# Kernel optimization log

Measured on AMD Instinct MI355X. Metric: run time of the kernel, lower is better.

The kernel has to match this reference:

```python
import jax, jax.numpy as jnp
import numpy as np

B, N, C = 4, 4096, 64
K1, K2 = 4, 6
MLP1 = [128, 64, 64]
MLP2 = [128, 64]
EPS = 1e-5


def _sqdist(a, b):
    # a: [B,N,3], b: [B,M,3] -> [B,N,M]
    return (jnp.sum(a * a, -1)[:, :, None] + jnp.sum(b * b, -1)[:, None, :]
            - 2.0 * jnp.einsum('bnc,bmc->bnm', a, b))


def _knn_idx(k, xyz, new_xyz):
    # matches knn_point: topk of -square_distance(new_xyz, xyz)
    _, idx = jax.lax.top_k(-_sqdist(new_xyz, xyz), k)
    return idx  # [B,S,k]


def _gather(points, idx):
    # index_points: points [B,N,C], idx [B,S,K] -> [B,S,K,C]
    return jax.vmap(lambda p, i: p[i])(points, idx)


def _conv_bn_relu(x, w, g, b):
    # 1x1 Conv2d (no bias) + BatchNorm2d (train mode) + ReLU, channels-last
    y = jnp.einsum('bnkc,oc->bnko', x, w)
    m = jnp.mean(y, axis=(0, 1, 2), keepdims=True)
    v = jnp.var(y, axis=(0, 1, 2), keepdims=True)
    return jax.nn.relu((y - m) * jax.lax.rsqrt(v + EPS) * g + b)


def _quat_mul(a, b):
    # Hamilton product, matches mul_q_point ordering
    aw, ax, ay, az = a[..., 0], a[..., 1], a[..., 2], a[..., 3]
    bw, bx, by, bz = b[..., 0], b[..., 1], b[..., 2], b[..., 3]
    return jnp.stack([
        aw * bw - ax * bx - ay * by - az * bz,
        aw * bx + ax * bw + ay * bz - az * by,
        aw * by - ax * bz + ay * bw + az * bx,
        aw * bz + ax * by - ay * bx + az * bw], axis=-1)


def _inv_q(q):
    n2 = jnp.sum(q * q, -1, keepdims=True) + 1e-10
    return jnp.concatenate([q[..., :1], -q[..., 1:]], -1) / n2


def _qrot(q, v):
    # rotate points v [B,M,3] by quaternion q [B,4] via q * (0,v) * q^-1
    vq = jnp.concatenate([jnp.zeros(v.shape[:-1] + (1,), v.dtype), v], -1)
    qb = q[:, None, :]
    return _quat_mul(_quat_mul(qb, vq), _inv_q(q)[:, None, :])[..., 1:]


def setup_inputs() -> dict:
    key = jax.random.key(0)
    ks = jax.random.split(key, 32)

    def rn(i, shape, s=1.0):
        return jax.random.normal(ks[i], shape, jnp.float32) * s

    inp = {
        'pos1': rn(0, (B, N, 3)),
        'pos2': rn(1, (B, N, 3)),
        'feat1': rn(2, (B, N, C)),
        'feat2': rn(3, (B, N, C)),
        'q_coarse': rn(4, (B, 4)),
        't_coarse': rn(5, (B, 3)),
    }
    c1 = [2 * C + 3] + MLP1
    for i in range(len(MLP1)):
        inp['w1_%d' % i] = rn(6 + i, (c1[i + 1], c1[i]), 0.1)
        inp['g1_%d' % i] = jnp.ones((c1[i + 1],), jnp.float32)
        inp['b1_%d' % i] = jnp.zeros((c1[i + 1],), jnp.float32)
    c2 = [MLP1[-1] + C + 3] + MLP2
    for i in range(len(MLP2)):
        inp['w2_%d' % i] = rn(12 + i, (c2[i + 1], c2[i]), 0.1)
        inp['g2_%d' % i] = jnp.ones((c2[i + 1],), jnp.float32)
        inp['b2_%d' % i] = jnp.zeros((c2[i + 1],), jnp.float32)
    inp['wq'] = rn(20, (4, MLP2[-1]), 0.01)
    inp['bq'] = jnp.zeros((4,), jnp.float32)
    inp['wt'] = rn(21, (3, MLP2[-1]), 0.01)
    inp['bt'] = jnp.zeros((3,), jnp.float32)
    return inp


def reference(pos1, pos2, feat1, feat2, q_coarse, t_coarse,
              w1_0, g1_0, b1_0, w1_1, g1_1, b1_1, w1_2, g1_2, b1_2,
              w2_0, g2_0, b2_0, w2_1, g2_1, b2_1, wq, bq, wt, bt):
    # warp pos1 by the coarse pose (q, t)
    pos1_w = _qrot(q_coarse, pos1) + t_coarse[:, None, :]

    # cross-cloud KNN grouping (FlowEmbedding first stage)
    idx2 = _knn_idx(K2, pos2, pos1_w)                      # [B,N,K2]
    xd2 = _gather(pos2, idx2) - pos1_w[:, :, None, :]      # [B,N,K2,3]
    f2g = _gather(feat2, idx2)                             # [B,N,K2,C]
    f1r = jnp.broadcast_to(feat1[:, :, None, :], (B, N, K2, C))
    x = jnp.concatenate([xd2, f2g, f1r], -1)               # [B,N,K2,131]
    for w, g, b in ((w1_0, g1_0, b1_0), (w1_1, g1_1, b1_1), (w1_2, g1_2, b1_2)):
        x = _conv_bn_relu(x, w, g, b)
    fe = jnp.sum(x, axis=2)                                # [B,N,64] sum pool over neighbors

    # self KNN grouping (FlowEmbedding second stage)
    idx1 = _knn_idx(K1, pos1_w, pos1_w)                    # [B,N,K1]
    xd1 = _gather(pos1_w, idx1) - pos1_w[:, :, None, :]
    feg = _gather(fe, idx1)
    f1r2 = jnp.broadcast_to(feat1[:, :, None, :], (B, N, K1, C))
    x = jnp.concatenate([xd1, feg, f1r2], -1)              # [B,N,K1,131]
    for w, g, b in ((w2_0, g2_0, b2_0), (w2_1, g2_1, b2_1)):
        x = _conv_bn_relu(x, w, g, b)
    pooled = jnp.sum(jnp.sum(x, axis=2), axis=1)           # [B,64] sum pool

    # pose delta heads + quaternion composition
    q_det = pooled @ wq.T + bq
    q_det = q_det / (jnp.linalg.norm(q_det, axis=-1, keepdims=True) + 1e-10)
    t_det = pooled @ wt.T + bt
    q_new = _quat_mul(q_det, q_coarse)
    q_new = q_new / (jnp.linalg.norm(q_new, axis=-1, keepdims=True) + 1e-10)
    t_new = _qrot(q_det, t_coarse[:, None, :])[:, 0, :] + t_det
    return jnp.concatenate([q_new, t_new], -1)             # [B,7]
```

## Files before the change

### kernel.cpp

```cpp
#include <hip/hip_runtime.h>
#include <math.h>

#define B_ 4
#define N_ 4096
#define C_ 64
#define K1_ 4
#define K2_ 6
#define EPS_ 1e-5f
#define BN_ (B_ * N_)
#define NCH_ 16
#define CHP_ 256
#define STKD_ 16

typedef __attribute__((ext_vector_type(8))) short bf16x8;
typedef __attribute__((ext_vector_type(4))) float f32x4;
typedef __attribute__((ext_vector_type(2))) float f32x2;

__device__ __forceinline__ unsigned short f2bf(float f) {
  unsigned int u = __float_as_uint(f);
  unsigned int r = (u + 0x7fffu + ((u >> 16) & 1u)) >> 16;
  return (unsigned short)r;
}
__device__ __forceinline__ float bf2f(unsigned short u) {
  return __uint_as_float(((unsigned int)u) << 16);
}

__global__ __launch_bounds__(256) void k_init(
    const float* __restrict__ w1_0, const float* __restrict__ w1_1,
    const float* __restrict__ w1_2, const float* __restrict__ w2_0,
    const float* __restrict__ w2_1, unsigned short* __restrict__ Wf2a,
    unsigned short* __restrict__ Wf1a, unsigned short* __restrict__ Wfe,
    unsigned short* __restrict__ Wf1b, unsigned short* __restrict__ wb1,
    unsigned short* __restrict__ wb2, unsigned short* __restrict__ wb4,
    const float* __restrict__ pos1, const float* __restrict__ pos2,
    const float* __restrict__ qc, const float* __restrict__ tc,
    float* __restrict__ posw, float4* __restrict__ pts4w, float4* __restrict__ pairW,
    float4* __restrict__ pairP) {
  int t = blockIdx.x * 256 + threadIdx.x;
  int m = blockIdx.y;
  if (m < 7) {
    switch (m) {
      case 0:
        if (t < 8192) Wf2a[t] = f2bf(w1_0[(t >> 6) * 131 + 3 + (t & 63)]);
        break;
      case 1:
        if (t < 8192) Wf1a[t] = f2bf(w1_0[(t >> 6) * 131 + 67 + (t & 63)]);
        break;
      case 2:
        if (t < 8192) Wfe[t] = f2bf(w2_0[(t >> 6) * 131 + 3 + (t & 63)]);
        break;
      case 3:
        if (t < 8192) Wf1b[t] = f2bf(w2_0[(t >> 6) * 131 + 67 + (t & 63)]);
        break;
      case 4:
        if (t < 8192) wb1[t] = f2bf(w1_1[t]);
        break;
      case 5:
        if (t < 4096) wb2[t] = f2bf(w1_2[t]);
        break;
      default:
        if (t < 8192) wb4[t] = f2bf(w2_1[t]);
        break;
    }
    return;
  }
  if (t >= BN_) return;
  int b = t / N_;
  float qw = qc[b * 4 + 0], qx = qc[b * 4 + 1], qy = qc[b * 4 + 2], qz = qc[b * 4 + 3];
  float vx = pos1[t * 3 + 0], vy = pos1[t * 3 + 1], vz = pos1[t * 3 + 2];
  float aw = -(qx * vx + qy * vy + qz * vz);
  float ax = qw * vx + qy * vz - qz * vy;
  float ay = qw * vy - qx * vz + qz * vx;
  float az = qw * vz + qx * vy - qy * vx;
  float n2 = qw * qw + qx * qx + qy * qy + qz * qz + 1e-10f;
  float bw = qw / n2, bx = -qx / n2, by = -qy / n2, bz = -qz / n2;
  float rx = aw * bx + ax * bw + ay * bz - az * by;
  float ry = aw * by - ax * bz + ay * bw + az * bx;
  float rz = aw * bz + ax * by - ay * bx + az * bw;
  rx += tc[b * 3 + 0];
  ry += tc[b * 3 + 1];
  rz += tc[b * 3 + 2];
  posw[t * 3 + 0] = rx;
  posw[t * 3 + 1] = ry;
  posw[t * 3 + 2] = rz;
  float rw2 = rx * rx + ry * ry + rz * rz;
  pts4w[t] = make_float4(rx, ry, rz, rw2);
  int p = t >> 1, h = t & 1;
  float* bwp = (float*)&pairW[(size_t)2 * p];
  bwp[0 + h] = rx; bwp[2 + h] = ry; bwp[4 + h] = rz; bwp[6 + h] = rw2;
  float px = pos2[t * 3 + 0], py = pos2[t * 3 + 1], pz = pos2[t * 3 + 2];
  float pw2 = px * px + py * py + pz * pz;
  float* bpp = (float*)&pairP[(size_t)2 * p];
  bpp[0 + h] = px; bpp[2 + h] = py; bpp[4 + h] = pz; bpp[6 + h] = pw2;
}

__device__ __forceinline__ void ins6i(int (&kd)[6], int k) {
  int x = k;
#pragma unroll
  for (int u = 0; u < 6; ++u) {
    int lo = min(kd[u], x);
    x = max(kd[u], x);
    kd[u] = lo;
  }
}

__global__ __launch_bounds__(256) void k_knn2(const float4* __restrict__ pts4w,
                                              const float4* __restrict__ pairW,
                                              const float4* __restrict__ pairP,
                                              int* __restrict__ outK) {
  __shared__ int st[STKD_][256];
  int tid = threadIdx.x;
  int b = blockIdx.z & 3;
  int which = blockIdx.z >> 2;
  const f32x4* __restrict__ PT =
      (const f32x4*)((which ? pairW : pairP) + (size_t)b * N_ + blockIdx.y * CHP_);
  int base = blockIdx.y * CHP_;
  int n = blockIdx.x * 256 + tid;
  float4 qv = pts4w[(size_t)b * N_ + n];
  f32x2 qq2 = (f32x2)(qv.w);
  f32x2 m2x = (f32x2)(-2.f * qv.x);
  f32x2 m2y = (f32x2)(-2.f * qv.y);
  f32x2 m2z = (f32x2)(-2.f * qv.z);
  int kd[6];
#pragma unroll
  for (int t = 0; t < 6; ++t) kd[t] = 0x7fffffff;
  int kbd5 = 0x7fffffff;
  int ptr = 0;
  for (int jj = 0; jj < CHP_; jj += 4) {
    f32x4 e0 = PT[jj + 0];
    f32x4 e1 = PT[jj + 1];
    f32x4 e2 = PT[jj + 2];
    f32x4 e3 = PT[jj + 3];
    f32x2 d01 = __builtin_elementwise_fma(
        m2x, e0.xy,
        __builtin_elementwise_fma(m2y, e0.zw,
                                  __builtin_elementwise_fma(m2z, e1.xy, e1.zw + qq2)));
    f32x2 d23 = __builtin_elementwise_fma(
        m2x, e2.xy,
        __builtin_elementwise_fma(m2y, e2.zw,
                                  __builtin_elementwise_fma(m2z, e3.xy, e3.zw + qq2)));
    int j0 = base + jj;
    int k0 = (int)((__float_as_uint(d01.x) & 0xFFFFF000u) | (unsigned)(j0 + 0));
    int k1 = (int)((__float_as_uint(d01.y) & 0xFFFFF000u) | (unsigned)(j0 + 1));
    int k2 = (int)((__float_as_uint(d23.x) & 0xFFFFF000u) | (unsigned)(j0 + 2));
    int k3 = (int)((__float_as_uint(d23.y) & 0xFFFFF000u) | (unsigned)(j0 + 3));
    st[ptr][tid] = k0;
    ptr += (k0 < kbd5) ? 1 : 0;
    st[ptr][tid] = k1;
    ptr += (k1 < kbd5) ? 1 : 0;
    st[ptr][tid] = k2;
    ptr += (k2 < kbd5) ? 1 : 0;
    st[ptr][tid] = k3;
    ptr += (k3 < kbd5) ? 1 : 0;
    if (__ballot(ptr >= STKD_ - 4)) {
      for (int i = 0; i < ptr; ++i) ins6i(kd, st[i][tid]);
      ptr = 0;
      kbd5 = kd[5];
    }
  }
  for (int i = 0; i < ptr; ++i) ins6i(kd, st[i][tid]);
  size_t ob =
      ((size_t)which * BN_ * NCH_ + (size_t)(b * N_ + n) * NCH_ + blockIdx.y) * 6;
#pragma unroll
  for (int t = 0; t < 6; ++t) outK[ob + t] = kd[t];
}

__global__ __launch_bounds__(64) void k_knn2_merge(const int* __restrict__ inK,
                                                   int* __restrict__ idx2,
                                                   int* __restrict__ idx1) {
  int t = blockIdx.x * 64 + threadIdx.x;
  if (t >= 2 * BN_) return;
  int which = (t >= BN_) ? 1 : 0;
  int qi = t - which * BN_;
  int kd[6];
#pragma unroll
  for (int u = 0; u < 6; ++u) kd[u] = 0x7fffffff;
  size_t ib = ((size_t)which * BN_ + qi) * NCH_ * 6;
  for (int c = 0; c < NCH_ * 6; ++c) ins6i(kd, inK[ib + c]);
  if (which) {
#pragma unroll
    for (int u = 0; u < K1_; ++u) idx1[(size_t)qi * K1_ + u] = kd[u] & 0xFFF;
  } else {
#pragma unroll
    for (int u = 0; u < K2_; ++u) idx2[(size_t)qi * K2_ + u] = kd[u] & 0xFFF;
  }
}

__device__ __forceinline__ void proj_mfma_tail(const unsigned short* Xs, int tid,
                                               int row0,
                                               const unsigned short* __restrict__ Wb,
                                               float* __restrict__ dst) {
  constexpr int SP = 72;
  int l = tid & 63, wv = tid >> 6;
  int lm = l & 15, quad = l >> 4;
  int n0 = wv * 32;
  f32x4 acc[4][2];
#pragma unroll
  for (int rt = 0; rt < 4; ++rt)
#pragma unroll
    for (int ct = 0; ct < 2; ++ct) acc[rt][ct] = (f32x4)(0.f);
#pragma unroll
  for (int k0 = 0; k0 < 64; k0 += 32) {
    bf16x8 a[4], b[2];
#pragma unroll
    for (int rt = 0; rt < 4; ++rt)
      a[rt] = *(const bf16x8*)&Xs[(rt * 16 + lm) * SP + k0 + quad * 8];
#pragma unroll
    for (int ct = 0; ct < 2; ++ct)
      b[ct] = *(const bf16x8*)&Wb[(size_t)(n0 + ct * 16 + lm) * 64 + k0 + quad * 8];
#pragma unroll
    for (int rt = 0; rt < 4; ++rt)
#pragma unroll
      for (int ct = 0; ct < 2; ++ct)
        acc[rt][ct] =
            __builtin_amdgcn_mfma_f32_16x16x32_bf16(a[rt], b[ct], acc[rt][ct], 0, 0, 0);
  }
#pragma unroll
  for (int rt = 0; rt < 4; ++rt)
#pragma unroll
    for (int ct = 0; ct < 2; ++ct)
#pragma unroll
      for (int r = 0; r < 4; ++r) {
        int row = row0 + rt * 16 + quad * 4 + r;
        dst[(size_t)row * 128 + n0 + ct * 16 + lm] = acc[rt][ct][r];
      }
}

__global__ __launch_bounds__(256) void k_proj(
    const float* __restrict__ s0, const unsigned short* __restrict__ w0,
    float* __restrict__ d0, const float* __restrict__ s1,
    const unsigned short* __restrict__ w1, float* __restrict__ d1,
    const float* __restrict__ s2, const unsigned short* __restrict__ w2,
    float* __restrict__ d2) {
  const float* src;
  const unsigned short* Wb;
  float* dst;
  switch (blockIdx.y) {
    case 0: src = s0; Wb = w0; dst = d0; break;
    case 1: src = s1; Wb = w1; dst = d1; break;
    default: src = s2; Wb = w2; dst = d2; break;
  }
  constexpr int SP = 72;
  __shared__ unsigned short Xs[64 * SP];
  int tid = threadIdx.x;
  int row0 = blockIdx.x * 64;
  for (int e = tid; e < 64 * 16; e += 256) {
    int r = e >> 4, s = e & 15;
    float4 v = *(const float4*)&src[(size_t)(row0 + r) * 64 + s * 4];
    ushort4 o;
    o.x = f2bf(v.x); o.y = f2bf(v.y); o.z = f2bf(v.z); o.w = f2bf(v.w);
    *(ushort4*)&Xs[r * SP + s * 4] = o;
  }
  __syncthreads();
  proj_mfma_tail(Xs, tid, row0, Wb, dst);
}

__global__ __launch_bounds__(256) void k_feproj(const unsigned short* __restrict__ y3,
                                                const float* __restrict__ stat,
                                                const float* __restrict__ g,
                                                const float* __restrict__ bb,
                                                const unsigned short* __restrict__ Wfe,
                                                float* __restrict__ Pfe) {
  constexpr int SP = 72;
  __shared__ unsigned short Xs[64 * SP];
  __shared__ float scl[C_], shf[C_];
  int tid = threadIdx.x;
  if (tid < C_) {
    int c = tid;
    float s = 0.f, s2 = 0.f;
#pragma unroll
    for (int u = 0; u < 8; ++u) {
      s += stat[c * 8 + u];
      s2 += stat[C_ * 8 + c * 8 + u];
    }
    const float invM = 1.f / (float)(BN_ * K2_);
    float m = s * invM;
    float v = s2 * invM - m * m;
    float sc = g[c] * rsqrtf(v + EPS_);
    scl[c] = sc;
    shf[c] = bb[c] - m * sc;
  }
  __syncthreads();
  int row0 = blockIdx.x * 64;
  for (int e = tid; e < 64 * 16; e += 256) {
    int r = e >> 4, s = e & 15;
    size_t base = ((size_t)(row0 + r) * K2_) * C_ + s * 4;
    float a0 = 0.f, a1 = 0.f, a2 = 0.f, a3 = 0.f;
#pragma unroll
    for (int k = 0; k < K2_; ++k) {
      ushort4 u = *(const ushort4*)&y3[base + (size_t)k * C_];
      a0 += fmaxf(fmaf(bf2f(u.x), scl[s * 4 + 0], shf[s * 4 + 0]), 0.f);
      a1 += fmaxf(fmaf(bf2f(u.y), scl[s * 4 + 1], shf[s * 4 + 1]), 0.f);
      a2 += fmaxf(fmaf(bf2f(u.z), scl[s * 4 + 2], shf[s * 4 + 2]), 0.f);
      a3 += fmaxf(fmaf(bf2f(u.w), scl[s * 4 + 3], shf[s * 4 + 3]), 0.f);
    }
    ushort4 o;
    o.x = f2bf(a0); o.y = f2bf(a1); o.z = f2bf(a2); o.w = f2bf(a3);
    *(ushort4*)&Xs[r * SP + s * 4] = o;
  }
  __syncthreads();
  proj_mfma_tail(Xs, tid, row0, Wfe, Pfe);
}

template <int KNN>
__global__ __launch_bounds__(256) void k_asm(
    const float* __restrict__ Wfull,
    const float* __restrict__ posP, const float* __restrict__ posw,
    const float* __restrict__ Pj, const float* __restrict__ Pn,
    const int* __restrict__ idx, unsigned short* __restrict__ yout,
    float* __restrict__ statOut) {
  __shared__ float Wx[3][128];
  __shared__ float red[16][128];
  int tid = threadIdx.x;
  if (tid < 128) {
    Wx[0][tid] = Wfull[tid * 131 + 0];
    Wx[1][tid] = Wfull[tid * 131 + 1];
    Wx[2][tid] = Wfull[tid * 131 + 2];
  }
  __syncthreads();
  int cg = tid & 15, rg = tid >> 4;
  int c0 = cg * 8;
  int row0 = blockIdx.x * 128 + rg * 8;
  float wx0[8], wx1[8], wx2[8];
#pragma unroll
  for (int u = 0; u < 8; ++u) {
    wx0[u] = Wx[0][c0 + u];
    wx1[u] = Wx[1][c0 + u];
    wx2[u] = Wx[2][c0 + u];
  }
  float s1[8], s2[8];
#pragma unroll
  for (int u = 0; u < 8; ++u) { s1[u] = 0.f; s2[u] = 0.f; }
#pragma unroll
  for (int i = 0; i < 8; ++i) {
    int row = row0 + i;
    int g = row / KNN;
    int bb = g >> 12;
    int j = idx[row];
    int gj = (bb << 12) + j;
    float xd0 = posP[(size_t)gj * 3 + 0] - posw[(size_t)g * 3 + 0];
    float xd1 = posP[(size_t)gj * 3 + 1] - posw[(size_t)g * 3 + 1];
    float xd2 = posP[(size_t)gj * 3 + 2] - posw[(size_t)g * 3 + 2];
    const float* pj = &Pj[(size_t)gj * 128 + c0];
    const float* pn = &Pn[(size_t)g * 128 + c0];
    float4 a0 = *(const float4*)&pj[0];
    float4 a1 = *(const float4*)&pj[4];
    float4 b0 = *(const float4*)&pn[0];
    float4 b1 = *(const float4*)&pn[4];
    float y[8];
    y[0] = a0.x + b0.x; y[1] = a0.y + b0.y; y[2] = a0.z + b0.z; y[3] = a0.w + b0.w;
    y[4] = a1.x + b1.x; y[5] = a1.y + b1.y; y[6] = a1.z + b1.z; y[7] = a1.w + b1.w;
    ushort4 o0, o1;
    unsigned short ob[8];
#pragma unroll
    for (int u = 0; u < 8; ++u) {
      float v = y[u];
      v = fmaf(xd0, wx0[u], v);
      v = fmaf(xd1, wx1[u], v);
      v = fmaf(xd2, wx2[u], v);
      s1[u] += v;
      s2[u] = fmaf(v, v, s2[u]);
      ob[u] = f2bf(v);
    }
    o0.x = ob[0]; o0.y = ob[1]; o0.z = ob[2]; o0.w = ob[3];
    o1.x = ob[4]; o1.y = ob[5]; o1.z = ob[6]; o1.w = ob[7];
    *(ushort4*)&yout[(size_t)row * 128 + c0] = o0;
    *(ushort4*)&yout[(size_t)row * 128 + c0 + 4] = o1;
  }
  int slot = blockIdx.x & 7;
#pragma unroll
  for (int u = 0; u < 8; ++u) red[rg][c0 + u] = s1[u];
  __syncthreads();
  if (tid < 128) {
    float s = 0.f;
#pragma unroll
    for (int r = 0; r < 16; ++r) s += red[r][tid];
    atomicAdd(&statOut[tid * 8 + slot], s);
  }
  __syncthreads();
#pragma unroll
  for (int u = 0; u < 8; ++u) red[rg][c0 + u] = s2[u];
  __syncthreads();
  if (tid < 128) {
    float s = 0.f;
#pragma unroll
    for (int r = 0; r < 16; ++r) s += red[r][tid];
    atomicAdd(&statOut[128 * 8 + tid * 8 + slot], s);
  }
}

template <int CIN, int COUT, int KP>
__global__ __launch_bounds__(256) void k_layer_mfma(
    const unsigned short* __restrict__ Wb,
    const unsigned short* __restrict__ yprev,
    const float* __restrict__ statPrev, const float* __restrict__ gPrev,
    const float* __restrict__ bPrev, float prevInvM,
    unsigned short* __restrict__ yout,
    float* __restrict__ statOut) {
  constexpr int SP = KP + 8;
  constexpr int CST = COUT + 8;
  constexpr int CT = COUT / 16;
  constexpr int NK = KP / 32;
  __shared__ unsigned short Xs[64 * SP];
  __shared__ float scl[CIN];
  __shared__ float shf[CIN];
  __shared__ float redS[8][COUT];

  int tid = threadIdx.x;
  int row0 = blockIdx.x * 64;

  for (int c = tid; c < CIN; c += 256) {
    float s = 0.f, s2 = 0.f;
#pragma unroll
    for (int u = 0; u < 8; ++u) {
      s += statPrev[c * 8 + u];
      s2 += statPrev[CIN * 8 + c * 8 + u];
    }
    float m = s * prevInvM;
    float v = s2 * prevInvM - m * m;
    float sc = gPrev[c] * rsqrtf(v + EPS_);
    scl[c] = sc;
    shf[c] = bPrev[c] - m * sc;
  }
  __syncthreads();
  constexpr int S4 = KP / 4;
  for (int e = tid; e < 64 * S4; e += 256) {
    int r = e / S4, s = e - r * S4;
    int row = row0 + r;
    ushort4 u = *(const ushort4*)&yprev[(size_t)row * CIN + s * 4];
    ushort4 o;
    o.x = f2bf(fmaxf(fmaf(bf2f(u.x), scl[s * 4 + 0], shf[s * 4 + 0]), 0.f));
    o.y = f2bf(fmaxf(fmaf(bf2f(u.y), scl[s * 4 + 1], shf[s * 4 + 1]), 0.f));
    o.z = f2bf(fmaxf(fmaf(bf2f(u.z), scl[s * 4 + 2], shf[s * 4 + 2]), 0.f));
    o.w = f2bf(fmaxf(fmaf(bf2f(u.w), scl[s * 4 + 3], shf[s * 4 + 3]), 0.f));
    *(ushort4*)&Xs[r * SP + s * 4] = o;
  }
  __syncthreads();

  int l = tid & 63, wv = tid >> 6;
  int lm = l & 15, quad = l >> 4;

  const unsigned short* wbase = &Wb[(size_t)lm * KP + quad * 8];
  const unsigned short* arow = &Xs[(wv * 16 + lm) * SP + quad * 8];

  bf16x8 Breg[NK][CT];
#pragma unroll
  for (int kk = 0; kk < NK; ++kk)
#pragma unroll
    for (int ct = 0; ct < CT; ++ct)
      Breg[kk][ct] = *(const bf16x8*)&wbase[(size_t)ct * 16 * KP + kk * 32];

  f32x4 acc[CT];
#pragma unroll
  for (int ct = 0; ct < CT; ++ct) acc[ct] = (f32x4)(0.f);
#pragma unroll
  for (int kk = 0; kk < NK; ++kk) {
    bf16x8 a = *(const bf16x8*)&arow[kk * 32];
#pragma unroll
    for (int ct = 0; ct < CT; ++ct)
      acc[ct] = __builtin_amdgcn_mfma_f32_16x16x32_bf16(a, Breg[kk][ct], acc[ct], 0, 0, 0);
  }

#pragma unroll
  for (int ct = 0; ct < CT; ++ct) {
    float s1 = 0.f, s2 = 0.f;
#pragma unroll
    for (int r = 0; r < 4; ++r) {
      float v = acc[ct][r];
      s1 += v;
      s2 += v * v;
    }
    s1 += __shfl_xor(s1, 16);
    s1 += __shfl_xor(s1, 32);
    s2 += __shfl_xor(s2, 16);
    s2 += __shfl_xor(s2, 32);
    if (quad == 0) {
      int col = ct * 16 + lm;
      redS[wv][col] = s1;
      redS[4 + wv][col] = s2;
    }
  }
  __syncthreads();
  int slot = blockIdx.x & 7;
  if (tid < COUT) {
    float s = redS[0][tid] + redS[1][tid] + redS[2][tid] + redS[3][tid];
    atomicAdd(&statOut[tid * 8 + slot], s);
  } else if (tid < 2 * COUT) {
    int c = tid - COUT;
    float s = redS[4][c] + redS[5][c] + redS[6][c] + redS[7][c];
    atomicAdd(&statOut[COUT * 8 + c * 8 + slot], s);
  }

  __syncthreads();
  unsigned short* Ys = Xs;
#pragma unroll
  for (int ct = 0; ct < CT; ++ct)
#pragma unroll
    for (int r = 0; r < 4; ++r)
      Ys[(wv * 16 + quad * 4 + r) * CST + ct * 16 + lm] = f2bf(acc[ct][r]);
  __syncthreads();
  constexpr int S8 = COUT / 8;
  for (int e = tid; e < 64 * S8; e += 256) {
    int r = e / S8, c0 = (e - r * S8) * 8;
    uint4 v = *(const uint4*)&Ys[r * CST + c0];
    *(uint4*)&yout[((size_t)(row0 + r)) * COUT + c0] = v;
  }
}

__global__ __launch_bounds__(256) void k_pooled(const unsigned short* __restrict__ y5,
                                                const float* __restrict__ stat,
                                                const float* __restrict__ g,
                                                const float* __restrict__ bb,
                                                float* __restrict__ pooled) {
  __shared__ float scl[C_], shf[C_];
  __shared__ float red[4][C_];
  if (threadIdx.x < C_) {
    int c = threadIdx.x;
    float s = 0.f, s2 = 0.f;
#pragma unroll
    for (int u = 0; u < 8; ++u) {
      s += stat[c * 8 + u];
      s2 += stat[C_ * 8 + c * 8 + u];
    }
    const float invM = 1.f / (float)(BN_ * K1_);
    float m = s * invM;
    float v = s2 * invM - m * m;
    float sc = g[c] * rsqrtf(v + EPS_);
    scl[c] = sc;
    shf[c] = bb[c] - m * sc;
  }
  __syncthreads();
  int c = threadIdx.x & 63;
  int rs = threadIdx.x >> 6;
  int row0 = blockIdx.x * 64;
  int b = row0 / (N_ * K1_);
  float s = 0.f;
  for (int i = 0; i < 16; ++i) {
    int row = row0 + rs * 16 + i;
    s += fmaxf(fmaf(bf2f(y5[(size_t)row * C_ + c]), scl[c], shf[c]), 0.f);
  }
  red[rs][c] = s;
  __syncthreads();
  if (threadIdx.x < C_) {
    float t2 = red[0][c] + red[1][c] + red[2][c] + red[3][c];
    atomicAdd(&pooled[(b * C_ + c) * 8 + (blockIdx.x & 7)], t2);
  }
}

__global__ void k_final(const float* __restrict__ pooled, const float* __restrict__ wq,
                        const float* __restrict__ bq, const float* __restrict__ wt,
                        const float* __restrict__ bt, const float* __restrict__ qc,
                        const float* __restrict__ tc, float* __restrict__ out) {
  int b = threadIdx.x;
  if (b >= B_) return;
  float P[C_];
#pragma unroll
  for (int c = 0; c < C_; ++c) {
    float s = 0.f;
#pragma unroll
    for (int u = 0; u < 8; ++u) s += pooled[(b * C_ + c) * 8 + u];
    P[c] = s;
  }
  float qd[4];
#pragma unroll
  for (int i = 0; i < 4; ++i) {
    float s = bq[i];
#pragma unroll
    for (int c = 0; c < C_; ++c) s = fmaf(P[c], wq[i * C_ + c], s);
    qd[i] = s;
  }
  float td[3];
#pragma unroll
  for (int i = 0; i < 3; ++i) {
    float s = bt[i];
#pragma unroll
    for (int c = 0; c < C_; ++c) s = fmaf(P[c], wt[i * C_ + c], s);
    td[i] = s;
  }
  float nq = sqrtf(qd[0] * qd[0] + qd[1] * qd[1] + qd[2] * qd[2] + qd[3] * qd[3]) + 1e-10f;
#pragma unroll
  for (int i = 0; i < 4; ++i) qd[i] /= nq;
  float cw = qc[b * 4 + 0], cx = qc[b * 4 + 1], cyy = qc[b * 4 + 2], cz = qc[b * 4 + 3];
  float qnw = qd[0] * cw - qd[1] * cx - qd[2] * cyy - qd[3] * cz;
  float qnx = qd[0] * cx + qd[1] * cw + qd[2] * cz - qd[3] * cyy;
  float qny = qd[0] * cyy - qd[1] * cz + qd[2] * cw + qd[3] * cx;
  float qnz = qd[0] * cz + qd[1] * cyy - qd[2] * cx + qd[3] * cw;
  float nn = sqrtf(qnw * qnw + qnx * qnx + qny * qny + qnz * qnz) + 1e-10f;
  float vx = tc[b * 3 + 0], vy = tc[b * 3 + 1], vz = tc[b * 3 + 2];
  float aw = -(qd[1] * vx + qd[2] * vy + qd[3] * vz);
  float ax = qd[0] * vx + qd[2] * vz - qd[3] * vy;
  float ay = qd[0] * vy - qd[1] * vz + qd[3] * vx;
  float az = qd[0] * vz + qd[1] * vy - qd[2] * vx;
  float n2 = qd[0] * qd[0] + qd[1] * qd[1] + qd[2] * qd[2] + qd[3] * qd[3] + 1e-10f;
  float bw = qd[0] / n2, bx = -qd[1] / n2, by = -qd[2] / n2, bz = -qd[3] / n2;
  float rx = aw * bx + ax * bw + ay * bz - az * by;
  float ry = aw * by - ax * bz + ay * bw + az * bx;
  float rz = aw * bz + ax * by - ay * bx + az * bw;
  out[b * 7 + 0] = qnw / nn;
  out[b * 7 + 1] = qnx / nn;
  out[b * 7 + 2] = qny / nn;
  out[b * 7 + 3] = qnz / nn;
  out[b * 7 + 4] = rx + td[0];
  out[b * 7 + 5] = ry + td[1];
  out[b * 7 + 6] = rz + td[2];
}

extern "C" void kernel_launch(void* const* d_in, const int* in_sizes, int n_in,
                              void* d_out, int out_size, void* d_ws, size_t ws_size,
                              hipStream_t stream) {
  const float* pos1 = (const float*)d_in[0];
  const float* pos2 = (const float*)d_in[1];
  const float* feat1 = (const float*)d_in[2];
  const float* feat2 = (const float*)d_in[3];
  const float* qc = (const float*)d_in[4];
  const float* tc = (const float*)d_in[5];
  const float* w1_0 = (const float*)d_in[6];
  const float* g1_0 = (const float*)d_in[7];
  const float* b1_0 = (const float*)d_in[8];
  const float* w1_1 = (const float*)d_in[9];
  const float* g1_1 = (const float*)d_in[10];
  const float* b1_1 = (const float*)d_in[11];
  const float* w1_2 = (const float*)d_in[12];
  const float* g1_2 = (const float*)d_in[13];
  const float* b1_2 = (const float*)d_in[14];
  const float* w2_0 = (const float*)d_in[15];
  const float* g2_0 = (const float*)d_in[16];
  const float* b2_0 = (const float*)d_in[17];
  const float* w2_1 = (const float*)d_in[18];
  const float* g2_1 = (const float*)d_in[19];
  const float* b2_1 = (const float*)d_in[20];
  const float* wq = (const float*)d_in[21];
  const float* bq = (const float*)d_in[22];
  const float* wt = (const float*)d_in[23];
  const float* bt = (const float*)d_in[24];

  float* ws = (float*)d_ws;
  const size_t off_posw = 0;
  const size_t off_stat = 49152;
  const size_t off_pool = 57344;
  const size_t off_idx2 = 59392;
  const size_t off_idx1 = 157696;
  const size_t off_wb = 223232;
  const size_t off_pts4w = 249856;
  const size_t off_pairW = 315392;
  const size_t off_pairP = 380928;
  const size_t off_P2a = 446464;
  const size_t off_P1a = 2543616;
  const size_t off_P1b = 4640768;
  const size_t off_Pfe = 6737920;
  const size_t off_yA = 8835072;
  const size_t off_yB = 15126528;

  float* posw = ws + off_posw;
  float* stat0 = ws + off_stat;
  float* stat1 = stat0 + 2048;
  float* stat2 = stat1 + 1024;
  float* stat3 = stat2 + 1024;
  float* stat4 = stat3 + 2048;
  float* pooled = ws + off_pool;
  int* idx2 = (int*)(ws + off_idx2);
  int* idx1 = (int*)(ws + off_idx1);
  unsigned short* Wf2a = (unsigned short*)(ws + off_wb);
  unsigned short* Wf1a = Wf2a + 8192;
  unsigned short* Wfe = Wf1a + 8192;
  unsigned short* Wf1b = Wfe + 8192;
  unsigned short* wb1 = Wf1b + 8192;
  unsigned short* wb2 = wb1 + 8192;
  unsigned short* wb4 = wb2 + 4096;
  float4* pts4w = (float4*)(ws + off_pts4w);
  float4* pairW = (float4*)(ws + off_pairW);
  float4* pairP = (float4*)(ws + off_pairP);
  float* P2a = ws + off_P2a;
  float* P1a = ws + off_P1a;
  float* P1b = ws + off_P1b;
  float* Pfe = ws + off_Pfe;
  unsigned short* yA = (unsigned short*)(ws + off_yA);
  unsigned short* yB = (unsigned short*)(ws + off_yB);
  int* knnK = (int*)yA;

  hipMemsetAsync(ws + off_stat, 0, (8192 + 2048) * sizeof(float), stream);

  k_init<<<dim3(64, 8), 256, 0, stream>>>(w1_0, w1_1, w1_2, w2_0, w2_1, Wf2a, Wf1a,
                                          Wfe, Wf1b, wb1, wb2, wb4, pos1, pos2, qc, tc,
                                          posw, pts4w, pairW, pairP);

  k_knn2<<<dim3(N_ / 256, NCH_, 2 * B_), 256, 0, stream>>>(pts4w, pairW, pairP, knnK);
  k_knn2_merge<<<dim3(2 * BN_ / 64), 64, 0, stream>>>(knnK, idx2, idx1);

  k_proj<<<dim3(256, 3), 256, 0, stream>>>(feat2, Wf2a, P2a, feat1, Wf1a, P1a, feat1,
                                           Wf1b, P1b);
  k_asm<K2_><<<dim3(98304 / 128), 256, 0, stream>>>(w1_0, pos2, posw, P2a, P1a, idx2,
                                                    yA, stat0);
  k_layer_mfma<128, 64, 128><<<dim3(1536), 256, 0, stream>>>(
      wb1, yA, stat0, g1_0, b1_0, 1.f / 98304.f, yB, stat1);
  k_layer_mfma<64, 64, 64><<<dim3(1536), 256, 0, stream>>>(
      wb2, yB, stat1, g1_1, b1_1, 1.f / 98304.f, yA, stat2);
  k_feproj<<<dim3(256), 256, 0, stream>>>(yA, stat2, g1_2, b1_2, Wfe, Pfe);
  k_asm<K1_><<<dim3(65536 / 128), 256, 0, stream>>>(w2_0, posw, posw, Pfe, P1b, idx1,
                                                    yA, stat3);
  k_layer_mfma<128, 64, 128><<<dim3(1024), 256, 0, stream>>>(
      wb4, yA, stat3, g2_0, b2_0, 1.f / 65536.f, yB, stat4);
  k_pooled<<<dim3(65536 / 64), 256, 0, stream>>>(yB, stat4, g2_1, b2_1, pooled);
  k_final<<<dim3(1), 64, 0, stream>>>(pooled, wq, bq, wt, bt, qc, tc, (float*)d_out);
}
```

Measured before the change: 390.4 us.

## Fuse KNN, merge and feature projection into one kernel with last-block merge

Result: slower. 655.2 us (+67.8%).

```diff
diff --git a/kernel.cpp b/kernel.cpp
--- a/kernel.cpp
+++ b/kernel.cpp
@@ -35,7 +35,7 @@
     const float* __restrict__ pos1, const float* __restrict__ pos2,
     const float* __restrict__ qc, const float* __restrict__ tc,
     float* __restrict__ posw, float4* __restrict__ pts4w, float4* __restrict__ pairW,
-    float4* __restrict__ pairP) {
+    float4* __restrict__ pairP, float* __restrict__ zbase) {
   int t = blockIdx.x * 256 + threadIdx.x;
   int m = blockIdx.y;
   if (m < 7) {
@@ -62,6 +62,10 @@
         if (t < 8192) wb4[t] = f2bf(w2_1[t]);
         break;
     }
+    return;
+  }
+  if (m == 8) {
+    if (t < 10368) zbase[t] = 0.f;
     return;
   }
   if (t >= BN_) return;
@@ -104,18 +108,87 @@
   }
 }
 
-__global__ __launch_bounds__(256) void k_knn2(const float4* __restrict__ pts4w,
-                                              const float4* __restrict__ pairW,
-                                              const float4* __restrict__ pairP,
-                                              int* __restrict__ outK) {
+__device__ __forceinline__ void proj_mfma_tail(const unsigned short* Xs, int tid,
+                                               int row0,
+                                               const unsigned short* __restrict__ Wb,
+                                               float* __restrict__ dst) {
+  constexpr int SP = 72;
+  int l = tid & 63, wv = tid >> 6;
+  int lm = l & 15, quad = l >> 4;
+  int n0 = wv * 32;
+  f32x4 acc[4][2];
+#pragma unroll
+  for (int rt = 0; rt < 4; ++rt)
+#pragma unroll
+    for (int ct = 0; ct < 2; ++ct) acc[rt][ct] = (f32x4)(0.f);
+#pragma unroll
+  for (int k0 = 0; k0 < 64; k0 += 32) {
+    bf16x8 a[4], b[2];
+#pragma unroll
+    for (int rt = 0; rt < 4; ++rt)
+      a[rt] = *(const bf16x8*)&Xs[(rt * 16 + lm) * SP + k0 + quad * 8];
+#pragma unroll
+    for (int ct = 0; ct < 2; ++ct)
+      b[ct] = *(const bf16x8*)&Wb[(size_t)(n0 + ct * 16 + lm) * 64 + k0 + quad * 8];
+#pragma unroll
+    for (int rt = 0; rt < 4; ++rt)
+#pragma unroll
+      for (int ct = 0; ct < 2; ++ct)
+        acc[rt][ct] =
+            __builtin_amdgcn_mfma_f32_16x16x32_bf16(a[rt], b[ct], acc[rt][ct], 0, 0, 0);
+  }
+#pragma unroll
+  for (int rt = 0; rt < 4; ++rt)
+#pragma unroll
+    for (int ct = 0; ct < 2; ++ct)
+#pragma unroll
+      for (int r = 0; r < 4; ++r) {
+        int row = row0 + rt * 16 + quad * 4 + r;
+        dst[(size_t)row * 128 + n0 + ct * 16 + lm] = acc[rt][ct][r];
+      }
+}
+
+__global__ __launch_bounds__(256) void k_knnproj(
+    const float4* __restrict__ pts4w, const float4* __restrict__ pairW,
+    const float4* __restrict__ pairP, int* __restrict__ outK, int* __restrict__ cnt,
+    int* __restrict__ idx2, int* __restrict__ idx1, const float* __restrict__ feat2,
+    const unsigned short* __restrict__ Wf2a, float* __restrict__ P2a,
+    const float* __restrict__ feat1, const unsigned short* __restrict__ Wf1a,
+    float* __restrict__ P1a, const unsigned short* __restrict__ Wf1b,
+    float* __restrict__ P1b) {
   __shared__ int st[STKD_][256];
   int tid = threadIdx.x;
-  int b = blockIdx.z & 3;
-  int which = blockIdx.z >> 2;
+  int bid = blockIdx.x;
+  if (bid < 768) {
+    const float* src;
+    const unsigned short* Wb;
+    float* dst;
+    switch (bid >> 8) {
+      case 0: src = feat2; Wb = Wf2a; dst = P2a; break;
+      case 1: src = feat1; Wb = Wf1a; dst = P1a; break;
+      default: src = feat1; Wb = Wf1b; dst = P1b; break;
+    }
+    unsigned short* Xs = (unsigned short*)&st[0][0];
+    int row0 = (bid & 255) * 64;
+    for (int e = tid; e < 64 * 16; e += 256) {
+      int r = e >> 4, s = e & 15;
+      float4 v = *(const float4*)&src[(size_t)(row0 + r) * 64 + s * 4];
+      ushort4 o;
+      o.x = f2bf(v.x); o.y = f2bf(v.y); o.z = f2bf(v.z); o.w = f2bf(v.w);
+      *(ushort4*)&Xs[r * 72 + s * 4] = o;
+    }
+    __syncthreads();
+    proj_mfma_tail(Xs, tid, row0, Wb, dst);
+    return;
+  }
+  int kbid = bid - 768;
+  int x = kbid & 15, y = (kbid >> 4) & 15, z = kbid >> 8;
+  int b = z & 3;
+  int which = z >> 2;
   const f32x4* __restrict__ PT =
-      (const f32x4*)((which ? pairW : pairP) + (size_t)b * N_ + blockIdx.y * CHP_);
-  int base = blockIdx.y * CHP_;
-  int n = blockIdx.x * 256 + tid;
+      (const f32x4*)((which ? pairW : pairP) + (size_t)b * N_ + y * CHP_);
+  int base = y * CHP_;
+  int n = x * 256 + tid;
   float4 qv = pts4w[(size_t)b * N_ + n];
   f32x2 qq2 = (f32x2)(qv.w);
   f32x2 m2x = (f32x2)(-2.f * qv.x);
@@ -159,100 +232,32 @@
     }
   }
   for (int i = 0; i < ptr; ++i) ins6i(kd, st[i][tid]);
-  size_t ob =
-      ((size_t)which * BN_ * NCH_ + (size_t)(b * N_ + n) * NCH_ + blockIdx.y) * 6;
+  size_t ob = ((size_t)which * BN_ * NCH_ + (size_t)(b * N_ + n) * NCH_ + y) * 6;
 #pragma unroll
   for (int t = 0; t < 6; ++t) outK[ob + t] = kd[t];
-}
-
-__global__ __launch_bounds__(64) void k_knn2_merge(const int* __restrict__ inK,
-                                                   int* __restrict__ idx2,
-                                                   int* __restrict__ idx1) {
-  int t = blockIdx.x * 64 + threadIdx.x;
-  if (t >= 2 * BN_) return;
-  int which = (t >= BN_) ? 1 : 0;
-  int qi = t - which * BN_;
-  int kd[6];
-#pragma unroll
-  for (int u = 0; u < 6; ++u) kd[u] = 0x7fffffff;
-  size_t ib = ((size_t)which * BN_ + qi) * NCH_ * 6;
-  for (int c = 0; c < NCH_ * 6; ++c) ins6i(kd, inK[ib + c]);
-  if (which) {
-#pragma unroll
-    for (int u = 0; u < K1_; ++u) idx1[(size_t)qi * K1_ + u] = kd[u] & 0xFFF;
-  } else {
-#pragma unroll
-    for (int u = 0; u < K2_; ++u) idx2[(size_t)qi * K2_ + u] = kd[u] & 0xFFF;
-  }
-}
-
-__device__ __forceinline__ void proj_mfma_tail(const unsigned short* Xs, int tid,
-                                               int row0,
-                                               const unsigned short* __restrict__ Wb,
-                                               float* __restrict__ dst) {
-  constexpr int SP = 72;
-  int l = tid & 63, wv = tid >> 6;
-  int lm = l & 15, quad = l >> 4;
-  int n0 = wv * 32;
-  f32x4 acc[4][2];
-#pragma unroll
-  for (int rt = 0; rt < 4; ++rt)
-#pragma unroll
-    for (int ct = 0; ct < 2; ++ct) acc[rt][ct] = (f32x4)(0.f);
-#pragma unroll
-  for (int k0 = 0; k0 < 64; k0 += 32) {
-    bf16x8 a[4], b[2];
-#pragma unroll
-    for (int rt = 0; rt < 4; ++rt)
-      a[rt] = *(const bf16x8*)&Xs[(rt * 16 + lm) * SP + k0 + quad * 8];
-#pragma unroll
-    for (int ct = 0; ct < 2; ++ct)
-      b[ct] = *(const bf16x8*)&Wb[(size_t)(n0 + ct * 16 + lm) * 64 + k0 + quad * 8];
-#pragma unroll
-    for (int rt = 0; rt < 4; ++rt)
-#pragma unroll
-      for (int ct = 0; ct < 2; ++ct)
-        acc[rt][ct] =
-            __builtin_amdgcn_mfma_f32_16x16x32_bf16(a[rt], b[ct], acc[rt][ct], 0, 0, 0);
-  }
-#pragma unroll
-  for (int rt = 0; rt < 4; ++rt)
-#pragma unroll
-    for (int ct = 0; ct < 2; ++ct)
-#pragma unroll
-      for (int r = 0; r < 4; ++r) {
-        int row = row0 + rt * 16 + quad * 4 + r;
-        dst[(size_t)row * 128 + n0 + ct * 16 + lm] = acc[rt][ct][r];
-      }
-}
-
-__global__ __launch_bounds__(256) void k_proj(
-    const float* __restrict__ s0, const unsigned short* __restrict__ w0,
-    float* __restrict__ d0, const float* __restrict__ s1,
-    const unsigned short* __restrict__ w1, float* __restrict__ d1,
-    const float* __restrict__ s2, const unsigned short* __restrict__ w2,
-    float* __restrict__ d2) {
-  const float* src;
-  const unsigned short* Wb;
-  float* dst;
-  switch (blockIdx.y) {
-    case 0: src = s0; Wb = w0; dst = d0; break;
-    case 1: src = s1; Wb = w1; dst = d1; break;
-    default: src = s2; Wb = w2; dst = d2; break;
-  }
-  constexpr int SP = 72;
-  __shared__ unsigned short Xs[64 * SP];
-  int tid = threadIdx.x;
-  int row0 = blockIdx.x * 64;
-  for (int e = tid; e < 64 * 16; e += 256) {
-    int r = e >> 4, s = e & 15;
-    float4 v = *(const float4*)&src[(size_t)(row0 + r) * 64 + s * 4];
-    ushort4 o;
-    o.x = f2bf(v.x); o.y = f2bf(v.y); o.z = f2bf(v.z); o.w = f2bf(v.w);
-    *(ushort4*)&Xs[r * SP + s * 4] = o;
-  }
-  __syncthreads();
-  proj_mfma_tail(Xs, tid, row0, Wb, dst);
+
+  __syncthreads();
+  __threadfence();
+  if (tid == 0) st[0][0] = atomicAdd(&cnt[z * 16 + x], 1);
+  __syncthreads();
+  if (st[0][0] == 15) {
+    __threadfence();
+    int q = x * 256 + tid;
+    int km[6];
+#pragma unroll
+    for (int u = 0; u < 6; ++u) km[u] = 0x7fffffff;
+    size_t ib = ((size_t)which * BN_ + (size_t)b * N_ + q) * (NCH_ * 6);
+    for (int c = 0; c < NCH_ * 6; ++c) ins6i(km, outK[ib + c]);
+    if (which) {
+#pragma unroll
+      for (int u = 0; u < K1_; ++u)
+        idx1[((size_t)b * N_ + q) * K1_ + u] = km[u] & 0xFFF;
+    } else {
+#pragma unroll
+      for (int u = 0; u < K2_; ++u)
+        idx2[((size_t)b * N_ + q) * K2_ + u] = km[u] & 0xFFF;
+    }
+  }
 }
 
 __global__ __launch_bounds__(256) void k_feproj(const unsigned short* __restrict__ y3,
@@ -638,18 +643,19 @@
   const size_t off_posw = 0;
   const size_t off_stat = 49152;
   const size_t off_pool = 57344;
-  const size_t off_idx2 = 59392;
-  const size_t off_idx1 = 157696;
-  const size_t off_wb = 223232;
-  const size_t off_pts4w = 249856;
-  const size_t off_pairW = 315392;
-  const size_t off_pairP = 380928;
-  const size_t off_P2a = 446464;
-  const size_t off_P1a = 2543616;
-  const size_t off_P1b = 4640768;
-  const size_t off_Pfe = 6737920;
-  const size_t off_yA = 8835072;
-  const size_t off_yB = 15126528;
+  const size_t off_cnt = 59392;
+  const size_t off_idx2 = 59520;
+  const size_t off_idx1 = 157824;
+  const size_t off_wb = 223360;
+  const size_t off_pts4w = 249984;
+  const size_t off_pairW = 315520;
+  const size_t off_pairP = 381056;
+  const size_t off_P2a = 446592;
+  const size_t off_P1a = 2543744;
+  const size_t off_P1b = 4640896;
+  const size_t off_Pfe = 6738048;
+  const size_t off_yA = 8835200;
+  const size_t off_yB = 15126656;
 
   float* posw = ws + off_posw;
   float* stat0 = ws + off_stat;
@@ -658,6 +664,7 @@
   float* stat3 = stat2 + 1024;
   float* stat4 = stat3 + 2048;
   float* pooled = ws + off_pool;
+  int* cnt = (int*)(ws + off_cnt);
   int* idx2 = (int*)(ws + off_idx2);
   int* idx1 = (int*)(ws + off_idx1);
   unsigned short* Wf2a = (unsigned short*)(ws + off_wb);
@@ -678,17 +685,14 @@
   unsigned short* yB = (unsigned short*)(ws + off_yB);
   int* knnK = (int*)yA;
 
-  hipMemsetAsync(ws + off_stat, 0, (8192 + 2048) * sizeof(float), stream);
-
-  k_init<<<dim3(64, 8), 256, 0, stream>>>(w1_0, w1_1, w1_2, w2_0, w2_1, Wf2a, Wf1a,
+  k_init<<<dim3(64, 9), 256, 0, stream>>>(w1_0, w1_1, w1_2, w2_0, w2_1, Wf2a, Wf1a,
                                           Wfe, Wf1b, wb1, wb2, wb4, pos1, pos2, qc, tc,
-                                          posw, pts4w, pairW, pairP);
-
-  k_knn2<<<dim3(N_ / 256, NCH_, 2 * B_), 256, 0, stream>>>(pts4w, pairW, pairP, knnK);
-  k_knn2_merge<<<dim3(2 * BN_ / 64), 64, 0, stream>>>(knnK, idx2, idx1);
-
-  k_proj<<<dim3(256, 3), 256, 0, stream>>>(feat2, Wf2a, P2a, feat1, Wf1a, P1a, feat1,
-                                           Wf1b, P1b);
+                                          posw, pts4w, pairW, pairP, ws + off_stat);
+
+  k_knnproj<<<dim3(768 + 2048), 256, 0, stream>>>(pts4w, pairW, pairP, knnK, cnt, idx2,
+                                                  idx1, feat2, Wf2a, P2a, feat1, Wf1a,
+                                                  P1a, Wf1b, P1b);
+
   k_asm<K2_><<<dim3(98304 / 128), 256, 0, stream>>>(w1_0, pos2, posw, P2a, P1a, idx2,
                                                     yA, stat0);
   k_layer_mfma<128, 64, 128><<<dim3(1536), 256, 0, stream>>>(
```

## Fuse projection into KNN kernel, fold stat memset into init, retile layer MFMA

Applied to the files above, without the earlier changes.

Result: no change. 383.8 us (-1.7%).

```diff
diff --git a/kernel.cpp b/kernel.cpp
--- a/kernel.cpp
+++ b/kernel.cpp
@@ -35,7 +35,7 @@
     const float* __restrict__ pos1, const float* __restrict__ pos2,
     const float* __restrict__ qc, const float* __restrict__ tc,
     float* __restrict__ posw, float4* __restrict__ pts4w, float4* __restrict__ pairW,
-    float4* __restrict__ pairP) {
+    float4* __restrict__ pairP, float* __restrict__ zbase) {
   int t = blockIdx.x * 256 + threadIdx.x;
   int m = blockIdx.y;
   if (m < 7) {
@@ -62,6 +62,10 @@
         if (t < 8192) wb4[t] = f2bf(w2_1[t]);
         break;
     }
+    return;
+  }
+  if (m == 8) {
+    if (t < 10240) zbase[t] = 0.f;
     return;
   }
   if (t >= BN_) return;
@@ -104,18 +108,86 @@
   }
 }
 
-__global__ __launch_bounds__(256) void k_knn2(const float4* __restrict__ pts4w,
-                                              const float4* __restrict__ pairW,
-                                              const float4* __restrict__ pairP,
-                                              int* __restrict__ outK) {
+__device__ __forceinline__ void proj_mfma_tail(const unsigned short* Xs, int tid,
+                                               int row0,
+                                               const unsigned short* __restrict__ Wb,
+                                               float* __restrict__ dst) {
+  constexpr int SP = 72;
+  int l = tid & 63, wv = tid >> 6;
+  int lm = l & 15, quad = l >> 4;
+  int n0 = wv * 32;
+  f32x4 acc[4][2];
+#pragma unroll
+  for (int rt = 0; rt < 4; ++rt)
+#pragma unroll
+    for (int ct = 0; ct < 2; ++ct) acc[rt][ct] = (f32x4)(0.f);
+#pragma unroll
+  for (int k0 = 0; k0 < 64; k0 += 32) {
+    bf16x8 a[4], b[2];
+#pragma unroll
+    for (int rt = 0; rt < 4; ++rt)
+      a[rt] = *(const bf16x8*)&Xs[(rt * 16 + lm) * SP + k0 + quad * 8];
+#pragma unroll
+    for (int ct = 0; ct < 2; ++ct)
+      b[ct] = *(const bf16x8*)&Wb[(size_t)(n0 + ct * 16 + lm) * 64 + k0 + quad * 8];
+#pragma unroll
+    for (int rt = 0; rt < 4; ++rt)
+#pragma unroll
+      for (int ct = 0; ct < 2; ++ct)
+        acc[rt][ct] =
+            __builtin_amdgcn_mfma_f32_16x16x32_bf16(a[rt], b[ct], acc[rt][ct], 0, 0, 0);
+  }
+#pragma unroll
+  for (int rt = 0; rt < 4; ++rt)
+#pragma unroll
+    for (int ct = 0; ct < 2; ++ct)
+#pragma unroll
+      for (int r = 0; r < 4; ++r) {
+        int row = row0 + rt * 16 + quad * 4 + r;
+        dst[(size_t)row * 128 + n0 + ct * 16 + lm] = acc[rt][ct][r];
+      }
+}
+
+__global__ __launch_bounds__(256) void k_knnproj(
+    const float4* __restrict__ pts4w, const float4* __restrict__ pairW,
+    const float4* __restrict__ pairP, int* __restrict__ outK,
+    const float* __restrict__ feat2, const unsigned short* __restrict__ Wf2a,
+    float* __restrict__ P2a, const float* __restrict__ feat1,
+    const unsigned short* __restrict__ Wf1a, float* __restrict__ P1a,
+    const unsigned short* __restrict__ Wf1b, float* __restrict__ P1b) {
   __shared__ int st[STKD_][256];
   int tid = threadIdx.x;
-  int b = blockIdx.z & 3;
-  int which = blockIdx.z >> 2;
+  int bid = blockIdx.x;
+  if (bid < 768) {
+    const float* src;
+    const unsigned short* Wb;
+    float* dst;
+    switch (bid >> 8) {
+      case 0: src = feat2; Wb = Wf2a; dst = P2a; break;
+      case 1: src = feat1; Wb = Wf1a; dst = P1a; break;
+      default: src = feat1; Wb = Wf1b; dst = P1b; break;
+    }
+    unsigned short* Xs = (unsigned short*)&st[0][0];
+    int row0 = (bid & 255) * 64;
+    for (int e = tid; e < 64 * 16; e += 256) {
+      int r = e >> 4, s = e & 15;
+      float4 v = *(const float4*)&src[(size_t)(row0 + r) * 64 + s * 4];
+      ushort4 o;
+      o.x = f2bf(v.x); o.y = f2bf(v.y); o.z = f2bf(v.z); o.w = f2bf(v.w);
+      *(ushort4*)&Xs[r * 72 + s * 4] = o;
+    }
+    __syncthreads();
+    proj_mfma_tail(Xs, tid, row0, Wb, dst);
+    return;
+  }
+  int kbid = bid - 768;
+  int x = kbid & 15, y = (kbid >> 4) & 15, z = kbid >> 8;
+  int b = z & 3;
+  int which = z >> 2;
   const f32x4* __restrict__ PT =
-      (const f32x4*)((which ? pairW : pairP) + (size_t)b * N_ + blockIdx.y * CHP_);
-  int base = blockIdx.y * CHP_;
-  int n = blockIdx.x * 256 + tid;
+      (const f32x4*)((which ? pairW : pairP) + (size_t)b * N_ + y * CHP_);
+  int base = y * CHP_;
+  int n = x * 256 + tid;
   float4 qv = pts4w[(size_t)b * N_ + n];
   f32x2 qq2 = (f32x2)(qv.w);
   f32x2 m2x = (f32x2)(-2.f * qv.x);
@@ -159,8 +231,7 @@
     }
   }
   for (int i = 0; i < ptr; ++i) ins6i(kd, st[i][tid]);
-  size_t ob =
-      ((size_t)which * BN_ * NCH_ + (size_t)(b * N_ + n) * NCH_ + blockIdx.y) * 6;
+  size_t ob = ((size_t)which * BN_ * NCH_ + (size_t)(b * N_ + n) * NCH_ + y) * 6;
 #pragma unroll
   for (int t = 0; t < 6; ++t) outK[ob + t] = kd[t];
 }
@@ -184,75 +255,6 @@
 #pragma unroll
     for (int u = 0; u < K2_; ++u) idx2[(size_t)qi * K2_ + u] = kd[u] & 0xFFF;
   }
-}
-
-__device__ __forceinline__ void proj_mfma_tail(const unsigned short* Xs, int tid,
-                                               int row0,
-                                               const unsigned short* __restrict__ Wb,
-                                               float* __restrict__ dst) {
-  constexpr int SP = 72;
-  int l = tid & 63, wv = tid >> 6;
-  int lm = l & 15, quad = l >> 4;
-  int n0 = wv * 32;
-  f32x4 acc[4][2];
-#pragma unroll
-  for (int rt = 0; rt < 4; ++rt)
-#pragma unroll
-    for (int ct = 0; ct < 2; ++ct) acc[rt][ct] = (f32x4)(0.f);
-#pragma unroll
-  for (int k0 = 0; k0 < 64; k0 += 32) {
-    bf16x8 a[4], b[2];
-#pragma unroll
-    for (int rt = 0; rt < 4; ++rt)
-      a[rt] = *(const bf16x8*)&Xs[(rt * 16 + lm) * SP + k0 + quad * 8];
-#pragma unroll
-    for (int ct = 0; ct < 2; ++ct)
-      b[ct] = *(const bf16x8*)&Wb[(size_t)(n0 + ct * 16 + lm) * 64 + k0 + quad * 8];
-#pragma unroll
-    for (int rt = 0; rt < 4; ++rt)
-#pragma unroll
-      for (int ct = 0; ct < 2; ++ct)
-        acc[rt][ct] =
-            __builtin_amdgcn_mfma_f32_16x16x32_bf16(a[rt], b[ct], acc[rt][ct], 0, 0, 0);
-  }
-#pragma unroll
-  for (int rt = 0; rt < 4; ++rt)
-#pragma unroll
-    for (int ct = 0; ct < 2; ++ct)
-#pragma unroll
-      for (int r = 0; r < 4; ++r) {
-        int row = row0 + rt * 16 + quad * 4 + r;
-        dst[(size_t)row * 128 + n0 + ct * 16 + lm] = acc[rt][ct][r];
-      }
-}
-
-__global__ __launch_bounds__(256) void k_proj(
-    const float* __restrict__ s0, const unsigned short* __restrict__ w0,
-    float* __restrict__ d0, const float* __restrict__ s1,
-    const unsigned short* __restrict__ w1, float* __restrict__ d1,
-    const float* __restrict__ s2, const unsigned short* __restrict__ w2,
-    float* __restrict__ d2) {
-  const float* src;
-  const unsigned short* Wb;
-  float* dst;
-  switch (blockIdx.y) {
-    case 0: src = s0; Wb = w0; dst = d0; break;
-    case 1: src = s1; Wb = w1; dst = d1; break;
-    default: src = s2; Wb = w2; dst = d2; break;
-  }
-  constexpr int SP = 72;
-  __shared__ unsigned short Xs[64 * SP];
-  int tid = threadIdx.x;
-  int row0 = blockIdx.x * 64;
-  for (int e = tid; e < 64 * 16; e += 256) {
-    int r = e >> 4, s = e & 15;
-    float4 v = *(const float4*)&src[(size_t)(row0 + r) * 64 + s * 4];
-    ushort4 o;
-    o.x = f2bf(v.x); o.y = f2bf(v.y); o.z = f2bf(v.z); o.w = f2bf(v.w);
-    *(ushort4*)&Xs[r * SP + s * 4] = o;
-  }
-  __syncthreads();
-  proj_mfma_tail(Xs, tid, row0, Wb, dst);
 }
 
 __global__ __launch_bounds__(256) void k_feproj(const unsigned short* __restrict__ y3,
@@ -399,12 +401,10 @@
     float* __restrict__ statOut) {
   constexpr int SP = KP + 8;
   constexpr int CST = COUT + 8;
-  constexpr int CT = COUT / 16;
-  constexpr int NK = KP / 32;
+  constexpr int CT = COUT / 64;
   __shared__ unsigned short Xs[64 * SP];
   __shared__ float scl[CIN];
   __shared__ float shf[CIN];
-  __shared__ float redS[8][COUT];
 
   int tid = threadIdx.x;
   int row0 = blockIdx.x * 64;
@@ -439,65 +439,63 @@
 
   int l = tid & 63, wv = tid >> 6;
   int lm = l & 15, quad = l >> 4;
-
-  const unsigned short* wbase = &Wb[(size_t)lm * KP + quad * 8];
-  const unsigned short* arow = &Xs[(wv * 16 + lm) * SP + quad * 8];
-
-  bf16x8 Breg[NK][CT];
-#pragma unroll
-  for (int kk = 0; kk < NK; ++kk)
+  int n0 = wv * (COUT / 4);
+
+  f32x4 acc[4][CT];
+#pragma unroll
+  for (int rt = 0; rt < 4; ++rt)
+#pragma unroll
+    for (int ct = 0; ct < CT; ++ct) acc[rt][ct] = (f32x4)(0.f);
+
+#pragma unroll
+  for (int k0 = 0; k0 < KP; k0 += 32) {
+    bf16x8 a[4], b[CT];
+#pragma unroll
+    for (int rt = 0; rt < 4; ++rt)
+      a[rt] = *(const bf16x8*)&Xs[(rt * 16 + lm) * SP + k0 + quad * 8];
 #pragma unroll
     for (int ct = 0; ct < CT; ++ct)
-      Breg[kk][ct] = *(const bf16x8*)&wbase[(size_t)ct * 16 * KP + kk * 32];
-
-  f32x4 acc[CT];
-#pragma unroll
-  for (int ct = 0; ct < CT; ++ct) acc[ct] = (f32x4)(0.f);
-#pragma unroll
-  for (int kk = 0; kk < NK; ++kk) {
-    bf16x8 a = *(const bf16x8*)&arow[kk * 32];
-#pragma unroll
-    for (int ct = 0; ct < CT; ++ct)
-      acc[ct] = __builtin_amdgcn_mfma_f32_16x16x32_bf16(a, Breg[kk][ct], acc[ct], 0, 0, 0);
-  }
-
+      b[ct] = *(const bf16x8*)&Wb[(size_t)(n0 + ct * 16 + lm) * KP + k0 + quad * 8];
+#pragma unroll
+    for (int rt = 0; rt < 4; ++rt)
+#pragma unroll
+      for (int ct = 0; ct < CT; ++ct)
+        acc[rt][ct] =
+            __builtin_amdgcn_mfma_f32_16x16x32_bf16(a[rt], b[ct], acc[rt][ct], 0, 0, 0);
+  }
+
+  int slot = blockIdx.x & 7;
 #pragma unroll
   for (int ct = 0; ct < CT; ++ct) {
     float s1 = 0.f, s2 = 0.f;
 #pragma unroll
-    for (int r = 0; r < 4; ++r) {
-      float v = acc[ct][r];
-      s1 += v;
-      s2 += v * v;
-    }
+    for (int rt = 0; rt < 4; ++rt)
+#pragma unroll
+      for (int r = 0; r < 4; ++r) {
+        float v = acc[rt][ct][r];
+        s1 += v;
+        s2 += v * v;
+      }
     s1 += __shfl_xor(s1, 16);
     s1 += __shfl_xor(s1, 32);
     s2 += __shfl_xor(s2, 16);
     s2 += __shfl_xor(s2, 32);
     if (quad == 0) {
-      int col = ct * 16 + lm;
-      redS[wv][col] = s1;
-      redS[4 + wv][col] = s2;
-    }
-  }
-  __syncthreads();
-  int slot = blockIdx.x & 7;
-  if (tid < COUT) {
-    float s = redS[0][tid] + redS[1][tid] + redS[2][tid] + redS[3][tid];
-    atomicAdd(&statOut[tid * 8 + slot], s);
-  } else if (tid < 2 * COUT) {
-    int c = tid - COUT;
-    float s = redS[4][c] + redS[5][c] + redS[6][c] + redS[7][c];
-    atomicAdd(&statOut[COUT * 8 + c * 8 + slot], s);
+      int col = n0 + ct * 16 + lm;
+      atomicAdd(&statOut[col * 8 + slot], s1);
+      atomicAdd(&statOut[COUT * 8 + col * 8 + slot], s2);
+    }
   }
 
   __syncthreads();
   unsigned short* Ys = Xs;
 #pragma unroll
-  for (int ct = 0; ct < CT; ++ct)
-#pragma unroll
-    for (int r = 0; r < 4; ++r)
-      Ys[(wv * 16 + quad * 4 + r) * CST + ct * 16 + lm] = f2bf(acc[ct][r]);
+  for (int rt = 0; rt < 4; ++rt)
+#pragma unroll
+    for (int ct = 0; ct < CT; ++ct)
+#pragma unroll
+      for (int r = 0; r < 4; ++r)
+        Ys[(rt * 16 + quad * 4 + r) * CST + n0 + ct * 16 + lm] = f2bf(acc[rt][ct][r]);
   __syncthreads();
   constexpr int S8 = COUT / 8;
   for (int e = tid; e < 64 * S8; e += 256) {
@@ -678,17 +676,15 @@
   unsigned short* yB = (unsigned short*)(ws + off_yB);
   int* knnK = (int*)yA;
 
-  hipMemsetAsync(ws + off_stat, 0, (8192 + 2048) * sizeof(float), stream);
-
-  k_init<<<dim3(64, 8), 256, 0, stream>>>(w1_0, w1_1, w1_2, w2_0, w2_1, Wf2a, Wf1a,
+  k_init<<<dim3(64, 9), 256, 0, stream>>>(w1_0, w1_1, w1_2, w2_0, w2_1, Wf2a, Wf1a,
                                           Wfe, Wf1b, wb1, wb2, wb4, pos1, pos2, qc, tc,
-                                          posw, pts4w, pairW, pairP);
-
-  k_knn2<<<dim3(N_ / 256, NCH_, 2 * B_), 256, 0, stream>>>(pts4w, pairW, pairP, knnK);
+                                          posw, pts4w, pairW, pairP, ws + off_stat);
+
+  k_knnproj<<<dim3(768 + 2048), 256, 0, stream>>>(pts4w, pairW, pairP, knnK, feat2,
+                                                  Wf2a, P2a, feat1, Wf1a, P1a, Wf1b,
+                                                  P1b);
   k_knn2_merge<<<dim3(2 * BN_ / 64), 64, 0, stream>>>(knnK, idx2, idx1);
 
-  k_proj<<<dim3(256, 3), 256, 0, stream>>>(feat2, Wf2a, P2a, feat1, Wf1a, P1a, feat1,
-                                           Wf1b, P1b);
   k_asm<K2_><<<dim3(98304 / 128), 256, 0, stream>>>(w1_0, pos2, posw, P2a, P1a, idx2,
                                                     yA, stat0);
   k_layer_mfma<128, 64, 128><<<dim3(1536), 256, 0, stream>>>(
```
